# Optimization experiments

Hardware: AMD Instinct MI355X
Metric: run time of the kernel (lower is better)

The kernel has to match this reference:

```python
import jax, jax.numpy as jnp
import numpy as np

N_NODES = 10000
N_EDGES = 320000
N_GRAPHS = 16


def _sage_layer(h, src, dst, W_self, W_neigh, b):
    # DGL SAGEConv('mean'): out_i = h_i @ W_self + mean_{j in N_in(i)} h_j @ W_neigh + b
    msg_sum = jax.ops.segment_sum(h[src], dst, num_segments=N_NODES)
    deg = jax.ops.segment_sum(jnp.ones(src.shape[0], h.dtype), dst, num_segments=N_NODES)
    h_neigh = msg_sum / jnp.maximum(deg, 1.0)[:, None]
    return h @ W_self + h_neigh @ W_neigh + b


def _segment_mean(x, seg, num_segments):
    s = jax.ops.segment_sum(x, seg, num_segments=num_segments)
    c = jax.ops.segment_sum(jnp.ones(x.shape[0], x.dtype), seg, num_segments=num_segments)
    return s / jnp.maximum(c, 1.0)[:, None]


def setup_inputs() -> dict:
    key = jax.random.key(0)
    ks = jax.random.split(key, 16)
    d_in, d_h, n_cls = 256, 64, 2

    def glorot(k, shape):
        fan_in = shape[0]
        return jax.random.normal(k, shape, dtype=jnp.float32) / np.sqrt(fan_in)

    return {
        "feat": jax.random.normal(ks[0], (N_NODES, d_in), dtype=jnp.float32),
        "src": jax.random.randint(ks[1], (N_EDGES,), 0, N_NODES),
        "dst": jax.random.randint(ks[2], (N_EDGES,), 0, N_NODES),
        "graph_id": jnp.sort(jax.random.randint(ks[3], (N_NODES,), 0, N_GRAPHS)),
        "W_self1": glorot(ks[4], (d_in, d_h)),
        "W_neigh1": glorot(ks[5], (d_in, d_h)),
        "b1": jnp.zeros((d_h,), jnp.float32),
        "W_self2": glorot(ks[6], (d_h, d_h)),
        "W_neigh2": glorot(ks[7], (d_h, d_h)),
        "b2": jnp.zeros((d_h,), jnp.float32),
        "W_self3": glorot(ks[8], (d_h, d_h)),
        "W_neigh3": glorot(ks[9], (d_h, d_h)),
        "b3": jnp.zeros((d_h,), jnp.float32),
        "W_cls": glorot(ks[10], (d_h, n_cls)),
        "b_cls": jnp.zeros((n_cls,), jnp.float32),
    }


def reference(feat, src, dst, graph_id, W_self1, W_neigh1, b1, W_self2, W_neigh2, b2,
              W_self3, W_neigh3, b3, W_cls, b_cls):
    # layer 1 + relu (dropout is identity in eval mode)
    h = jax.nn.relu(_sage_layer(feat, src, dst, W_self1, W_neigh1, b1))
    # layer 2 + relu
    h = jax.nn.relu(_sage_layer(h, src, dst, W_self2, W_neigh2, b2))
    # layer 3 (no activation)
    h = _sage_layer(h, src, dst, W_self3, W_neigh3, b3)
    # dgl.mean_nodes readout per graph
    out_feat = _segment_mean(h, graph_id, N_GRAPHS)
    out = out_feat @ W_cls + b_cls
    return (out, out_feat, h)
```

## Files before the change

### kernel.cpp

```cpp
#include <hip/hip_runtime.h>


#define DH 64
#define NG 16
#define NSB 8
#define DTILES 32
#define MAXNPB 1250
#define CAP 32

__device__ __forceinline__ unsigned short f2bf(float f) {
    unsigned int u = __float_as_uint(f);
    unsigned int r = (u + 0x7FFFu + ((u >> 16) & 1u)) >> 16;
    return (unsigned short)r;
}
__device__ __forceinline__ float bfu(unsigned short v) {
    return __uint_as_float(((unsigned int)v) << 16);
}
__device__ __forceinline__ int deg8(const int* __restrict__ cnt8, int n) {
    const int4* cp = reinterpret_cast<const int4*>(&cnt8[n * NSB]);
    int4 c0 = cp[0], c1 = cp[1];
    return c0.x + c0.y + c0.z + c0.w + c1.x + c1.y + c1.z + c1.w;
}

__global__ __launch_bounds__(256) void gemm1_build_kernel(
    const float* __restrict__ X, const float* __restrict__ Ws_g,
    const float* __restrict__ Wn_g, const float* __restrict__ bias,
    float* __restrict__ S, unsigned short* __restrict__ P,
    float* __restrict__ Hn_out,
    const int* __restrict__ src, const int* __restrict__ dst,
    int* __restrict__ cnt8, int* __restrict__ es,
    int M, int E, int npb8, int gb) {
    constexpr int K = 256;
    int tid = threadIdx.x;

    if ((int)blockIdx.x >= gb) {
        int i = ((int)blockIdx.x - gb) * 256 + tid;
        if (i < E) {
            int s = src[i];
            int k = dst[i] * NSB + s / npb8;
            int p = atomicAdd(&cnt8[k], 1);
            if (p < CAP) es[(size_t)k * CAP + p] = s;
        }
        return;
    }

    __shared__ float Xs[64][68];
    __shared__ float Ws[64][68];
    __shared__ float Wn[64][68];
    int row0 = blockIdx.x * 64;
    int cx = tid & 15;
    int ry = tid >> 4;
    float acc_s[4][4] = {{0.f}};
    float acc_n[4][4] = {{0.f}};

    for (int kc = 0; kc < K; kc += 64) {
#pragma unroll
        for (int it = 0; it < 4; ++it) {
            int q = tid + 256 * it;
            int row = q >> 4;
            int k4 = (q & 15) * 4;
            float4 xv = make_float4(0.f, 0.f, 0.f, 0.f);
            int gr = row0 + row;
            if (gr < M)
                xv = *reinterpret_cast<const float4*>(&X[(size_t)gr * K + kc + k4]);
            *reinterpret_cast<float4*>(&Xs[row][k4]) = xv;
            float4 wv = *reinterpret_cast<const float4*>(&Ws_g[(size_t)(kc + row) * 64 + k4]);
            *reinterpret_cast<float4*>(&Ws[row][k4]) = wv;
            float4 nv = *reinterpret_cast<const float4*>(&Wn_g[(size_t)(kc + row) * 64 + k4]);
            *reinterpret_cast<float4*>(&Wn[row][k4]) = nv;
        }
        __syncthreads();
#pragma unroll 4
        for (int kk = 0; kk < 64; ++kk) {
            float av[4], bs[4], bn[4];
#pragma unroll
            for (int j = 0; j < 4; ++j) av[j] = Xs[ry * 4 + j][kk];
#pragma unroll
            for (int i = 0; i < 4; ++i) {
                bs[i] = Ws[kk][cx + 16 * i];
                bn[i] = Wn[kk][cx + 16 * i];
            }
#pragma unroll
            for (int j = 0; j < 4; ++j)
#pragma unroll
                for (int i = 0; i < 4; ++i) {
                    acc_s[j][i] += av[j] * bs[i];
                    acc_n[j][i] += av[j] * bn[i];
                }
        }
        __syncthreads();
    }

#pragma unroll
    for (int j = 0; j < 4; ++j) {
        int r = row0 + ry * 4 + j;
        if (r < M) {
#pragma unroll
            for (int i = 0; i < 4; ++i) {
                int col = cx + 16 * i;
                S[(size_t)r * DH + col] = acc_s[j][i] + bias[col];
                P[(size_t)r * DH + col] = f2bf(acc_n[j][i]);
                Hn_out[(size_t)r * DH + col] = 0.f;
            }
        }
    }
}

__global__ __launch_bounds__(256) void gemm_dual_kernel(
    const float* __restrict__ X, const float* __restrict__ Ws_g,
    const float* __restrict__ Wn_g, const float* __restrict__ bias,
    const float* __restrict__ Hn_in, const int* __restrict__ cnt8,
    float* __restrict__ S, unsigned short* __restrict__ P,
    float* __restrict__ Hn_out, int M) {
    constexpr int K = 64;
    __shared__ float Xs[64][68];
    __shared__ float Ws[64][68];
    __shared__ float Wn[64][68];
    int tid = threadIdx.x;
    int row0 = blockIdx.x * 64;
    int cx = tid & 15;
    int ry = tid >> 4;
    float acc_s[4][4] = {{0.f}};
    float acc_n[4][4] = {{0.f}};

    {
#pragma unroll
        for (int it = 0; it < 4; ++it) {
            int q = tid + 256 * it;
            int row = q >> 4;
            int k4 = (q & 15) * 4;
            float4 xv = make_float4(0.f, 0.f, 0.f, 0.f);
            int gr = row0 + row;
            if (gr < M) {
                xv = *reinterpret_cast<const float4*>(&X[(size_t)gr * K + k4]);
                float4 hv = *reinterpret_cast<const float4*>(&Hn_in[(size_t)gr * DH + k4]);
                float inv = 1.f / fmaxf((float)deg8(cnt8, gr), 1.f);
                xv.x = fmaxf(fmaf(hv.x, inv, xv.x), 0.f);
                xv.y = fmaxf(fmaf(hv.y, inv, xv.y), 0.f);
                xv.z = fmaxf(fmaf(hv.z, inv, xv.z), 0.f);
                xv.w = fmaxf(fmaf(hv.w, inv, xv.w), 0.f);
            }
            *reinterpret_cast<float4*>(&Xs[row][k4]) = xv;
            float4 wv = *reinterpret_cast<const float4*>(&Ws_g[(size_t)row * 64 + k4]);
            *reinterpret_cast<float4*>(&Ws[row][k4]) = wv;
            float4 nv = *reinterpret_cast<const float4*>(&Wn_g[(size_t)row * 64 + k4]);
            *reinterpret_cast<float4*>(&Wn[row][k4]) = nv;
        }
        __syncthreads();
#pragma unroll 4
        for (int kk = 0; kk < 64; ++kk) {
            float av[4], bs[4], bn[4];
#pragma unroll
            for (int j = 0; j < 4; ++j) av[j] = Xs[ry * 4 + j][kk];
#pragma unroll
            for (int i = 0; i < 4; ++i) {
                bs[i] = Ws[kk][cx + 16 * i];
                bn[i] = Wn[kk][cx + 16 * i];
            }
#pragma unroll
            for (int j = 0; j < 4; ++j)
#pragma unroll
                for (int i = 0; i < 4; ++i) {
                    acc_s[j][i] += av[j] * bs[i];
                    acc_n[j][i] += av[j] * bn[i];
                }
        }
        __syncthreads();
    }

#pragma unroll
    for (int j = 0; j < 4; ++j) {
        int r = row0 + ry * 4 + j;
        if (r < M) {
#pragma unroll
            for (int i = 0; i < 4; ++i) {
                int col = cx + 16 * i;
                S[(size_t)r * DH + col] = acc_s[j][i] + bias[col];
                P[(size_t)r * DH + col] = f2bf(acc_n[j][i]);
                Hn_out[(size_t)r * DH + col] = 0.f;
            }
        }
    }
}

__global__ __launch_bounds__(1024) void agg_kernel(
    const unsigned short* __restrict__ P, const int* __restrict__ cnt8,
    const int* __restrict__ es, float* __restrict__ Hn, int M, int npb8) {
    __shared__ __align__(16) unsigned short sP[MAXNPB * DH];
    int tid = threadIdx.x;
    int sb    = blockIdx.x & (NSB - 1);
    int dtile = blockIdx.x >> 3;
    int s0 = sb * npb8;
    int snodes = min(npb8, M - s0);

    {
        const uint4* gp = reinterpret_cast<const uint4*>(P + (size_t)s0 * DH);
        int cnt = snodes * 8;
        for (int j = tid; j < cnt; j += 1024)
            *reinterpret_cast<uint4*>(&sP[j * 8]) = gp[j];
    }
    __syncthreads();

    int lane = tid & 63, wid = tid >> 6;
    int dpb  = (M + DTILES - 1) / DTILES;
    int d0t  = dtile * dpb;
    int dend = min(d0t + dpb, M);

    for (int dstn = d0t + wid; dstn < dend; dstn += 16) {
        int key = dstn * NSB + sb;
        int cnt = min(cnt8[key], CAP);
        if (cnt == 0) continue;
        size_t base = (size_t)key * CAP;
        float acc = 0.f;
        int cmax = cnt - 1;
        for (int e = 0; e < cnt; e += 4) {
            int i0 = es[base + min(e + 0, cmax)] - s0;
            int i1 = es[base + min(e + 1, cmax)] - s0;
            int i2 = es[base + min(e + 2, cmax)] - s0;
            int i3 = es[base + min(e + 3, cmax)] - s0;
            float m1 = (e + 1 < cnt) ? 1.f : 0.f;
            float m2 = (e + 2 < cnt) ? 1.f : 0.f;
            float m3 = (e + 3 < cnt) ? 1.f : 0.f;
            float f0 = bfu(sP[(size_t)i0 * DH + lane]);
            float f1 = bfu(sP[(size_t)i1 * DH + lane]);
            float f2 = bfu(sP[(size_t)i2 * DH + lane]);
            float f3 = bfu(sP[(size_t)i3 * DH + lane]);
            acc += f0;
            acc = fmaf(m1, f1, acc);
            acc = fmaf(m2, f2, acc);
            acc = fmaf(m3, f3, acc);
        }
        atomicAdd(&Hn[(size_t)dstn * DH + lane], acc);
    }
}

__global__ __launch_bounds__(256) void finish_readout_kernel(
    const float* __restrict__ S, const float* __restrict__ Hn,
    const int* __restrict__ cnt8, const int* __restrict__ graph_id,
    float* __restrict__ H, float* __restrict__ gsum, float* __restrict__ gcnt,
    const float* __restrict__ Wc, const float* __restrict__ bc,
    float* __restrict__ out, float* __restrict__ out_feat,
    unsigned int* __restrict__ done, int M, int fb) {
    int tid  = threadIdx.x;
    int lane = tid & 63;
    int wv   = tid >> 6;
    {
        int wid = blockIdx.x * 4 + wv;
        int nw  = fb * 4;
        int cpw = (M + nw - 1) / nw;
        int n0 = wid * cpw, n1 = min(n0 + cpw, M);
        if (n0 < n1) {
            float acc = 0.f;
            int cnt = 0;
            int cur = graph_id[n0];
            for (int n = n0; n < n1; ++n) {
                int gid = graph_id[n];
                if (gid != cur) {
                    atomicAdd(&gsum[cur * DH + lane], acc);
                    if (lane == 0) atomicAdd(&gcnt[cur], (float)cnt);
                    acc = 0.f; cnt = 0; cur = gid;
                }
                float inv = 1.f / fmaxf((float)deg8(cnt8, n), 1.f);
                size_t o = (size_t)n * DH + lane;
                float val = fmaf(Hn[o], inv, S[o]);
                H[o] = val;
                acc += val;
                ++cnt;
            }
            atomicAdd(&gsum[cur * DH + lane], acc);
            if (lane == 0) atomicAdd(&gcnt[cur], (float)cnt);
        }
    }

    __shared__ unsigned int s_ticket;
    __syncthreads();
    if (tid == 0) {
        __threadfence();
        s_ticket = __hip_atomic_fetch_add(done, 1u, __ATOMIC_ACQ_REL,
                                          __HIP_MEMORY_SCOPE_AGENT);
    }
    __syncthreads();
    if (s_ticket != (unsigned int)(fb - 1)) return;
    if (tid == 0) __threadfence();
    __syncthreads();

    __shared__ float ofs[NG][DH];
#pragma unroll
    for (int q = 0; q < 4; ++q) {
        int idx = tid + 256 * q;
        int g = idx >> 6, d = idx & 63;
        float of = gsum[idx] / fmaxf(gcnt[g], 1.0f);
        out_feat[idx] = of;
        ofs[g][d] = of;
    }
    __syncthreads();
    if (tid < NG * 2) {
        int gg = tid >> 1, cc = tid & 1;
        float accv = bc[cc];
#pragma unroll 8
        for (int dd = 0; dd < DH; ++dd) accv += ofs[gg][dd] * Wc[dd * 2 + cc];
        out[gg * 2 + cc] = accv;
    }
}

extern "C" void kernel_launch(void* const* d_in, const int* in_sizes, int n_in,
                              void* d_out, int out_size, void* d_ws, size_t ws_size,
                              hipStream_t stream) {
    const float* feat     = (const float*)d_in[0];
    const int*   src      = (const int*)d_in[1];
    const int*   dst      = (const int*)d_in[2];
    const int*   graph_id = (const int*)d_in[3];
    const float* Ws1 = (const float*)d_in[4];
    const float* Wn1 = (const float*)d_in[5];
    const float* b1  = (const float*)d_in[6];
    const float* Ws2 = (const float*)d_in[7];
    const float* Wn2 = (const float*)d_in[8];
    const float* b2  = (const float*)d_in[9];
    const float* Ws3 = (const float*)d_in[10];
    const float* Wn3 = (const float*)d_in[11];
    const float* b3  = (const float*)d_in[12];
    const float* Wc  = (const float*)d_in[13];
    const float* bc  = (const float*)d_in[14];

    const int M  = in_sizes[3];
    const int E  = in_sizes[1];
    const int M2 = M * NSB;
    const int npb8 = (M + NSB - 1) / NSB;

    float* out      = (float*)d_out;
    float* out_feat = out + NG * 2;
    float* Hbuf     = out_feat + NG * DH;

    char* w = (char*)d_ws;
    size_t off = 0;
    auto carve = [&](size_t bytes) {
        size_t o = off;
        off = (off + bytes + 255) & ~(size_t)255;
        return o;
    };
    int*   cnt8  = (int*)  (w + carve((size_t)M2 * 4));
    float* gsum  = (float*)(w + carve((size_t)NG * DH * 4));
    float* gcnt  = (float*)(w + carve((size_t)NG * 4));
    unsigned int* done = (unsigned int*)(w + carve(4));
    size_t zero_bytes = off;
    int*   es    = (int*)  (w + carve((size_t)M2 * CAP * 4));
    float* Sbuf  = (float*)(w + carve((size_t)M * DH * 4));
    unsigned short* Pbuf = (unsigned short*)(w + carve((size_t)M * DH * 2));
    float* Hn    = (float*)(w + carve((size_t)M * DH * 4));
    (void)ws_size; (void)n_in; (void)out_size;

    (void)hipMemsetAsync(d_ws, 0, zero_bytes, stream);

    int gb = (M + 63) / 64;
    int eb = (E + 255) / 256;
    int ab = NSB * DTILES;
    int fb = 160;

    gemm1_build_kernel<<<gb + eb, 256, 0, stream>>>(
        feat, Ws1, Wn1, b1, Sbuf, Pbuf, Hn,
        src, dst, cnt8, es, M, E, npb8, gb);
    agg_kernel<<<ab, 1024, 0, stream>>>(Pbuf, cnt8, es, Hn, M, npb8);

    gemm_dual_kernel<<<gb, 256, 0, stream>>>(
        Sbuf, Ws2, Wn2, b2, Hn, cnt8, Sbuf, Pbuf, Hn, M);
    agg_kernel<<<ab, 1024, 0, stream>>>(Pbuf, cnt8, es, Hn, M, npb8);

    gemm_dual_kernel<<<gb, 256, 0, stream>>>(
        Sbuf, Ws3, Wn3, b3, Hn, cnt8, Sbuf, Pbuf, Hn, M);
    agg_kernel<<<ab, 1024, 0, stream>>>(Pbuf, cnt8, es, Hn, M, npb8);

    finish_readout_kernel<<<fb, 256, 0, stream>>>(
        Sbuf, Hn, cnt8, graph_id, Hbuf, gsum, gcnt,
        Wc, bc, out, out_feat, done, M, fb);
}
```

Baseline: 249.1 us.

## Split GEMM K dimension across two thread groups with shared-memory reduction

Both GEMM kernels now launch 512 threads per block and split the reduction dimension between two 256-thread groups. Each group accumulates a partial 64x64 tile, and the partials are combined through shared memory before the epilogue. With only about 157 row blocks this doubles the threads working on the small GEMMs and halves each thread's serial k-loop. The cost is more shared memory per block (about 104KB in gemm1), an extra barrier and reduction pass, and half the threads sitting idle in the epilogue. The edge-bucketing part of gemm1 now also uses 512 threads per block.

```diff
diff --git a/kernel.cpp b/kernel.cpp
--- a/kernel.cpp
+++ b/kernel.cpp
@@ -7,6 +7,7 @@
 #define DTILES 32
 #define MAXNPB 1250
 #define CAP 32
+#define TILE_F 4352
 
 __device__ __forceinline__ unsigned short f2bf(float f) {
     unsigned int u = __float_as_uint(f);
@@ -22,7 +23,7 @@
     return c0.x + c0.y + c0.z + c0.w + c1.x + c1.y + c1.z + c1.w;
 }
 
-__global__ __launch_bounds__(256) void gemm1_build_kernel(
+__global__ __launch_bounds__(512) void gemm1_build_kernel(
     const float* __restrict__ X, const float* __restrict__ Ws_g,
     const float* __restrict__ Wn_g, const float* __restrict__ bias,
     float* __restrict__ S, unsigned short* __restrict__ P,
@@ -34,7 +35,7 @@
     int tid = threadIdx.x;
 
     if ((int)blockIdx.x >= gb) {
-        int i = ((int)blockIdx.x - gb) * 256 + tid;
+        int i = ((int)blockIdx.x - gb) * 512 + tid;
         if (i < E) {
             int s = src[i];
             int k = dst[i] * NSB + s / npb8;
@@ -44,41 +45,45 @@
         return;
     }
 
-    __shared__ float Xs[64][68];
-    __shared__ float Ws[64][68];
-    __shared__ float Wn[64][68];
-    int row0 = blockIdx.x * 64;
-    int cx = tid & 15;
-    int ry = tid >> 4;
+    __shared__ float smem[6 * TILE_F];
+    const int grp = tid >> 8;
+    const int t   = tid & 255;
+    const int cx = t & 15;
+    const int ry = t >> 4;
+    float* Xs  = smem + grp * 3 * TILE_F;
+    float* Wsm = Xs + TILE_F;
+    float* Wnm = Wsm + TILE_F;
+    const int row0 = blockIdx.x * 64;
     float acc_s[4][4] = {{0.f}};
     float acc_n[4][4] = {{0.f}};
 
-    for (int kc = 0; kc < K; kc += 64) {
+    for (int st = 0; st < 2; ++st) {
+        const int kc = grp * 128 + st * 64;
 #pragma unroll
         for (int it = 0; it < 4; ++it) {
-            int q = tid + 256 * it;
+            int q = t + 256 * it;
             int row = q >> 4;
             int k4 = (q & 15) * 4;
             float4 xv = make_float4(0.f, 0.f, 0.f, 0.f);
             int gr = row0 + row;
             if (gr < M)
                 xv = *reinterpret_cast<const float4*>(&X[(size_t)gr * K + kc + k4]);
-            *reinterpret_cast<float4*>(&Xs[row][k4]) = xv;
-            float4 wv = *reinterpret_cast<const float4*>(&Ws_g[(size_t)(kc + row) * 64 + k4]);
-            *reinterpret_cast<float4*>(&Ws[row][k4]) = wv;
-            float4 nv = *reinterpret_cast<const float4*>(&Wn_g[(size_t)(kc + row) * 64 + k4]);
-            *reinterpret_cast<float4*>(&Wn[row][k4]) = nv;
+            *reinterpret_cast<float4*>(&Xs[row * 68 + k4]) = xv;
+            *reinterpret_cast<float4*>(&Wsm[row * 68 + k4]) =
+                *reinterpret_cast<const float4*>(&Ws_g[(size_t)(kc + row) * 64 + k4]);
+            *reinterpret_cast<float4*>(&Wnm[row * 68 + k4]) =
+                *reinterpret_cast<const float4*>(&Wn_g[(size_t)(kc + row) * 64 + k4]);
         }
         __syncthreads();
 #pragma unroll 4
         for (int kk = 0; kk < 64; ++kk) {
             float av[4], bs[4], bn[4];
 #pragma unroll
-            for (int j = 0; j < 4; ++j) av[j] = Xs[ry * 4 + j][kk];
-#pragma unroll
-            for (int i = 0; i < 4; ++i) {
-                bs[i] = Ws[kk][cx + 16 * i];
-                bn[i] = Wn[kk][cx + 16 * i];
+            for (int j = 0; j < 4; ++j) av[j] = Xs[(ry * 4 + j) * 68 + kk];
+#pragma unroll
+            for (int i = 0; i < 4; ++i) {
+                bs[i] = Wsm[kk * 68 + cx + 16 * i];
+                bn[i] = Wnm[kk * 68 + cx + 16 * i];
             }
 #pragma unroll
             for (int j = 0; j < 4; ++j)
@@ -91,42 +96,67 @@
         __syncthreads();
     }
 
-#pragma unroll
-    for (int j = 0; j < 4; ++j) {
-        int r = row0 + ry * 4 + j;
-        if (r < M) {
-#pragma unroll
-            for (int i = 0; i < 4; ++i) {
-                int col = cx + 16 * i;
-                S[(size_t)r * DH + col] = acc_s[j][i] + bias[col];
-                P[(size_t)r * DH + col] = f2bf(acc_n[j][i]);
-                Hn_out[(size_t)r * DH + col] = 0.f;
-            }
-        }
-    }
-}
-
-__global__ __launch_bounds__(256) void gemm_dual_kernel(
+    float* flat = smem + 3 * TILE_F;
+    if (grp == 1) {
+        int o = t * 33;
+#pragma unroll
+        for (int j = 0; j < 4; ++j)
+#pragma unroll
+            for (int i = 0; i < 4; ++i) {
+                flat[o + j * 4 + i]      = acc_s[j][i];
+                flat[o + 16 + j * 4 + i] = acc_n[j][i];
+            }
+    }
+    __syncthreads();
+    if (grp == 0) {
+        int o = t * 33;
+#pragma unroll
+        for (int j = 0; j < 4; ++j)
+#pragma unroll
+            for (int i = 0; i < 4; ++i) {
+                acc_s[j][i] += flat[o + j * 4 + i];
+                acc_n[j][i] += flat[o + 16 + j * 4 + i];
+            }
+#pragma unroll
+        for (int j = 0; j < 4; ++j) {
+            int r = row0 + ry * 4 + j;
+            if (r < M) {
+#pragma unroll
+                for (int i = 0; i < 4; ++i) {
+                    int col = cx + 16 * i;
+                    S[(size_t)r * DH + col] = acc_s[j][i] + bias[col];
+                    P[(size_t)r * DH + col] = f2bf(acc_n[j][i]);
+                    Hn_out[(size_t)r * DH + col] = 0.f;
+                }
+            }
+        }
+    }
+}
+
+__global__ __launch_bounds__(512) void gemm_dual_kernel(
     const float* __restrict__ X, const float* __restrict__ Ws_g,
     const float* __restrict__ Wn_g, const float* __restrict__ bias,
     const float* __restrict__ Hn_in, const int* __restrict__ cnt8,
     float* __restrict__ S, unsigned short* __restrict__ P,
     float* __restrict__ Hn_out, int M) {
     constexpr int K = 64;
-    __shared__ float Xs[64][68];
-    __shared__ float Ws[64][68];
-    __shared__ float Wn[64][68];
+    __shared__ float smem[3 * TILE_F];
     int tid = threadIdx.x;
-    int row0 = blockIdx.x * 64;
-    int cx = tid & 15;
-    int ry = tid >> 4;
+    const int grp = tid >> 8;
+    const int t   = tid & 255;
+    const int cx = t & 15;
+    const int ry = t >> 4;
+    float* Xs  = smem;
+    float* Wsm = smem + TILE_F;
+    float* Wnm = smem + 2 * TILE_F;
+    const int row0 = blockIdx.x * 64;
     float acc_s[4][4] = {{0.f}};
     float acc_n[4][4] = {{0.f}};
 
     {
 #pragma unroll
-        for (int it = 0; it < 4; ++it) {
-            int q = tid + 256 * it;
+        for (int it = 0; it < 2; ++it) {
+            int q = tid + 512 * it;
             int row = q >> 4;
             int k4 = (q & 15) * 4;
             float4 xv = make_float4(0.f, 0.f, 0.f, 0.f);
@@ -140,22 +170,23 @@
                 xv.z = fmaxf(fmaf(hv.z, inv, xv.z), 0.f);
                 xv.w = fmaxf(fmaf(hv.w, inv, xv.w), 0.f);
             }
-            *reinterpret_cast<float4*>(&Xs[row][k4]) = xv;
-            float4 wv = *reinterpret_cast<const float4*>(&Ws_g[(size_t)row * 64 + k4]);
-            *reinterpret_cast<float4*>(&Ws[row][k4]) = wv;
-            float4 nv = *reinterpret_cast<const float4*>(&Wn_g[(size_t)row * 64 + k4]);
-            *reinterpret_cast<float4*>(&Wn[row][k4]) = nv;
+            *reinterpret_cast<float4*>(&Xs[row * 68 + k4]) = xv;
+            *reinterpret_cast<float4*>(&Wsm[row * 68 + k4]) =
+                *reinterpret_cast<const float4*>(&Ws_g[(size_t)row * 64 + k4]);
+            *reinterpret_cast<float4*>(&Wnm[row * 68 + k4]) =
+                *reinterpret_cast<const float4*>(&Wn_g[(size_t)row * 64 + k4]);
         }
         __syncthreads();
+        const int kk0 = grp * 32;
 #pragma unroll 4
-        for (int kk = 0; kk < 64; ++kk) {
+        for (int kk = kk0; kk < kk0 + 32; ++kk) {
             float av[4], bs[4], bn[4];
 #pragma unroll
-            for (int j = 0; j < 4; ++j) av[j] = Xs[ry * 4 + j][kk];
-#pragma unroll
-            for (int i = 0; i < 4; ++i) {
-                bs[i] = Ws[kk][cx + 16 * i];
-                bn[i] = Wn[kk][cx + 16 * i];
+            for (int j = 0; j < 4; ++j) av[j] = Xs[(ry * 4 + j) * 68 + kk];
+#pragma unroll
+            for (int i = 0; i < 4; ++i) {
+                bs[i] = Wsm[kk * 68 + cx + 16 * i];
+                bn[i] = Wnm[kk * 68 + cx + 16 * i];
             }
 #pragma unroll
             for (int j = 0; j < 4; ++j)
@@ -168,16 +199,37 @@
         __syncthreads();
     }
 
-#pragma unroll
-    for (int j = 0; j < 4; ++j) {
-        int r = row0 + ry * 4 + j;
-        if (r < M) {
-#pragma unroll
-            for (int i = 0; i < 4; ++i) {
-                int col = cx + 16 * i;
-                S[(size_t)r * DH + col] = acc_s[j][i] + bias[col];
-                P[(size_t)r * DH + col] = f2bf(acc_n[j][i]);
-                Hn_out[(size_t)r * DH + col] = 0.f;
+    if (grp == 1) {
+        int o = t * 33;
+#pragma unroll
+        for (int j = 0; j < 4; ++j)
+#pragma unroll
+            for (int i = 0; i < 4; ++i) {
+                smem[o + j * 4 + i]      = acc_s[j][i];
+                smem[o + 16 + j * 4 + i] = acc_n[j][i];
+            }
+    }
+    __syncthreads();
+    if (grp == 0) {
+        int o = t * 33;
+#pragma unroll
+        for (int j = 0; j < 4; ++j)
+#pragma unroll
+            for (int i = 0; i < 4; ++i) {
+                acc_s[j][i] += smem[o + j * 4 + i];
+                acc_n[j][i] += smem[o + 16 + j * 4 + i];
+            }
+#pragma unroll
+        for (int j = 0; j < 4; ++j) {
+            int r = row0 + ry * 4 + j;
+            if (r < M) {
+#pragma unroll
+                for (int i = 0; i < 4; ++i) {
+                    int col = cx + 16 * i;
+                    S[(size_t)r * DH + col] = acc_s[j][i] + bias[col];
+                    P[(size_t)r * DH + col] = f2bf(acc_n[j][i]);
+                    Hn_out[(size_t)r * DH + col] = 0.f;
+                }
             }
         }
     }
@@ -352,20 +404,20 @@
     (void)hipMemsetAsync(d_ws, 0, zero_bytes, stream);
 
     int gb = (M + 63) / 64;
-    int eb = (E + 255) / 256;
+    int eb = (E + 511) / 512;
     int ab = NSB * DTILES;
     int fb = 160;
 
-    gemm1_build_kernel<<<gb + eb, 256, 0, stream>>>(
+    gemm1_build_kernel<<<gb + eb, 512, 0, stream>>>(
         feat, Ws1, Wn1, b1, Sbuf, Pbuf, Hn,
         src, dst, cnt8, es, M, E, npb8, gb);
     agg_kernel<<<ab, 1024, 0, stream>>>(Pbuf, cnt8, es, Hn, M, npb8);
 
-    gemm_dual_kernel<<<gb, 256, 0, stream>>>(
+    gemm_dual_kernel<<<gb, 512, 0, stream>>>(
         Sbuf, Ws2, Wn2, b2, Hn, cnt8, Sbuf, Pbuf, Hn, M);
     agg_kernel<<<ab, 1024, 0, stream>>>(Pbuf, cnt8, es, Hn, M, npb8);
 
-    gemm_dual_kernel<<<gb, 256, 0, stream>>>(
+    gemm_dual_kernel<<<gb, 512, 0, stream>>>(
         Sbuf, Ws3, Wn3, b3, Hn, cnt8, Sbuf, Pbuf, Hn, M);
     agg_kernel<<<ab, 1024, 0, stream>>>(Pbuf, cnt8, es, Hn, M, npb8);
 
```

Measured after the change: 233.4 us (median of 2 runs). 1.07x faster.
